# Kernel tuning notes

Measured on AMD Instinct MI355X. Metric: run time of the kernel, lower is better.

Reference implementation:

```python
import jax, jax.numpy as jnp
import numpy as np

SHIFTS = (1, 2, 4, 8)


def _base_kernels():
    # 8 directional contrast kernels (center minus one neighbor), as in the torch module
    d1 = np.array([[[-1, 0, 0], [0, 1, 0], [0, 0, 0]],
                   [[0, -1, 0], [0, 1, 0], [0, 0, 0]],
                   [[0, 0, -1], [0, 1, 0], [0, 0, 0]],
                   [[0, 0, 0], [0, 1, -1], [0, 0, 0]]], dtype=np.float32)
    d2 = d1[:, ::-1, ::-1].copy()
    delta = np.concatenate([d1, d2], axis=0)            # (8,3,3) kernel*_1
    su0 = np.ones((3, 3), np.float32) / 8.0             # original kernel_su
    ce = np.zeros((3, 3), np.float32); ce[1, 1] = 1.0   # kernel_ce
    k2 = (delta - ce) * (9.0 / 8.0) + su0               # (8,3,3) kernel*_2
    su_f = su0 * (7.0 / 8.0); su_f[1, 1] = 1.0 / 8.0    # mutated kernel_su used for cen_x
    return jnp.asarray(delta), jnp.asarray(k2), jnp.asarray(su_f), jnp.asarray(ce)


def _dwconv(x, w, dil, groups):
    # depthwise 3x3 dilated conv, padding='same' (stride 1)
    return jax.lax.conv_general_dilated(
        x, w, window_strides=(1, 1), padding='SAME',
        rhs_dilation=(dil, dil),
        dimension_numbers=('NCHW', 'OIHW', 'NCHW'),
        feature_group_count=groups)


def setup_inputs() -> dict:
    key = jax.random.key(0)
    ks = jax.random.split(key, 6)
    B, C, Wd, Ht = 8, 16, 192, 192
    H, T, OC = 4, 64, 32
    hid = T // H  # 16
    return {
        'cen': jax.random.normal(ks[0], (B, C, Wd, Ht), jnp.float32),
        'wq': jax.random.normal(ks[1], (H, hid, C), jnp.float32) * 0.1,
        'wk': jax.random.normal(ks[2], (H, 8 * hid, 8 * C), jnp.float32) * 0.05,
        'wv': jax.random.normal(ks[3], (H, 8 * hid, 8 * C), jnp.float32) * 0.05,
        'sum_w': jnp.full((H, C), 0.5, jnp.float32),  # Parameter(ones)*0.5
        'w_out': jax.random.normal(ks[4], (OC, T), jnp.float32) * 0.1,
        'gamma': jnp.ones((OC,), jnp.float32),
        'beta': jnp.zeros((OC,), jnp.float32),
    }


def reference(cen, wq, wk, wv, sum_w, w_out, gamma, beta):
    delta, k2, su_f, ce = _base_kernels()
    B, C, Wd, Ht = cen.shape
    H = len(SHIFTS)
    hid = wq.shape[1]
    N = Wd * Ht  # self.area
    qs, ks_, vs = [], [], []
    for i, s in enumerate(SHIFTS):
        sw = sum_w[i]  # (C,) per-channel blend weight
        # center-smoothing kernel: kernel_su*(1-sw) + sw*kernel_ce
        w_cen = (su_f[None] * (1.0 - sw)[:, None, None]
                 + ce[None] * sw[:, None, None])[:, None]          # (C,1,3,3)
        cen_x = _dwconv(cen, w_cen, s, C)                           # (B,C,Wd,Ht)
        # 8 blended contrast kernels: k1*(1-sw) + k2*sw, per channel
        w_sur = (delta[None] * (1.0 - sw)[:, None, None, None]
                 + k2[None] * sw[:, None, None, None]).reshape(C * 8, 1, 3, 3)
        sur = _dwconv(cen, w_sur, s, C)                             # (B, C*8, Wd, Ht), channel-major
        # reorder to torch cat order: [k0 all C, k1 all C, ...]
        sur = sur.reshape(B, C, 8, Wd, Ht).transpose(0, 2, 1, 3, 4).reshape(B, 8 * C, Wd, Ht)
        qs.append(jnp.einsum('oc,bchw->bohw', wq[i], cen_x).reshape(B, hid, N))
        ks_.append(jnp.einsum('oc,bchw->bohw', wk[i], sur).reshape(B, 8 * hid, N))
        vs.append(jnp.einsum('oc,bchw->bohw', wv[i], sur).reshape(B, 8 * hid, N))
    Q = jnp.stack(qs, 1)   # (B,H,hid,N)
    K = jnp.stack(ks_, 1)  # (B,H,8*hid,N)
    V = jnp.stack(vs, 1)   # (B,H,8*hid,N)
    # F.normalize over spatial dim (channel attention)
    Qn = Q / jnp.maximum(jnp.linalg.norm(Q, axis=-1, keepdims=True), 1e-12)
    Kn = K / jnp.maximum(jnp.linalg.norm(K, axis=-1, keepdims=True), 1e-12)
    score = jnp.einsum('bhqn,bhkn->bhqk', Qn, Kn) / jnp.sqrt(jnp.float32(N))
    # InstanceNorm2d(num_heads), affine=False, biased var
    m = score.mean(axis=(-2, -1), keepdims=True)
    v = score.var(axis=(-2, -1), keepdims=True)
    score = (score - m) / jnp.sqrt(v + 1e-5)
    attn = jax.nn.softmax(score, axis=-1)
    out = jnp.einsum('bhqk,bhkn->bhqn', attn, V).reshape(B, H * hid, Wd, Ht)  # (B,T,Wd,Ht)
    # out_conv: 1x1 conv + BatchNorm2d (train-mode batch stats) + ReLU
    y = jnp.einsum('oc,bchw->bohw', w_out, out)
    mu = y.mean(axis=(0, 2, 3), keepdims=True)
    var = y.var(axis=(0, 2, 3), keepdims=True)
    y = (y - mu) / jnp.sqrt(var + 1e-5) * gamma[None, :, None, None] + beta[None, :, None, None]
    return jax.nn.relu(y)
```

## Files before the change

kernel.cpp:

```cpp
#include <hip/hip_runtime.h>
#include <hip/hip_bf16.h>

typedef __hip_bfloat16 bf16;
typedef unsigned short u16;
typedef u16 u16x8 __attribute__((ext_vector_type(8)));
typedef __bf16 bf16x8 __attribute__((ext_vector_type(8)));
typedef float f32x4 __attribute__((ext_vector_type(4)));

#define NPIX 36864
#define NTOT 9437184
#define BNPIX 294912.0f

__device__ __forceinline__ float cvt(float v){ return v; }
__device__ __forceinline__ float cvt(bf16 v){ return __bfloat162float(v); }
__device__ __forceinline__ void stv(float* p, float v){ *p = v; }
__device__ __forceinline__ void stv(bf16* p, float v){ *p = __float2bfloat16(v); }
__device__ __forceinline__ u16 f2us(float v){ bf16 b = __float2bfloat16(v); u16 u; __builtin_memcpy(&u,&b,2); return u; }
__device__ __forceinline__ float us2f(u16 v){ unsigned u = ((unsigned)v)<<16; float f; __builtin_memcpy(&f,&u,4); return f; }
__device__ __forceinline__ void fence(){ __builtin_amdgcn_sched_barrier(0); }

__constant__ int tA[45] = {0,0,0,0,0,0,0,0,0,4,4, 1,1,1,1,1,1,1,1,4,4,4, 2,2,2,2,2,2,2,5,5,5,5, 3,3,3,3,3,3,6,6,6,7,7,8};
__constant__ int tB[45] = {0,1,2,3,4,5,6,7,8,4,5, 1,2,3,4,5,6,7,8,6,7,8, 2,3,4,5,6,7,8,5,6,7,8, 3,4,5,6,7,8,6,7,8,7,8,8};

__global__ void k0_detect(const unsigned* __restrict__ gamma_raw, int* __restrict__ mode)
{
    if (threadIdx.x == 0) mode[0] = (gamma_raw[0] == 0x3F803F80u) ? 1 : 0;
}

struct K1S { u16 F[144*128]; };

__device__ __forceinline__ void flushU(const f32x4& v, int A, int B, float* __restrict__ g, int ln, int lg)
{
    #pragma unroll
    for (int r = 0; r < 4; ++r)
        atomicAdd(&g[(A*16 + lg*4 + r)*144 + B*16 + ln], v[r]);
}

template<typename T>
__device__ __forceinline__ void ldseg(const T* p, bool pred, float* o)
{
    if constexpr (sizeof(T) == 2){
        u16x8 v = {0,0,0,0,0,0,0,0};
        if (pred) v = *(const u16x8*)p;
        #pragma unroll
        for (int i = 0; i < 8; ++i) o[i] = us2f(v[i]);
    } else {
        float4 a = {0,0,0,0}, b = {0,0,0,0};
        if (pred){ a = ((const float4*)p)[0]; b = ((const float4*)p)[1]; }
        o[0]=a.x; o[1]=a.y; o[2]=a.z; o[3]=a.w; o[4]=b.x; o[5]=b.y; o[6]=b.z; o[7]=b.w;
    }
}

template<typename T, int S_>
__device__ __forceinline__ void k1_build(const T* __restrict__ cc, float swc, K1S& S,
                                         int bx, int ck, int glocal, int c, int gs)
{
    const int gg = (bx*6 + ck)*16 + glocal;
    const int row = gg/24;
    const int colb = (gg - row*24)*8;
    float w3[3][24];
    #pragma unroll
    for (int rr = 0; rr < 3; ++rr){
        int r2 = row + (rr-1)*S_;
        bool rok = (unsigned)r2 < 192u;
        const T* rp = cc + r2*192 + colb;
        ldseg(rp-8, rok && (colb != 0),   &w3[rr][0]);
        ldseg(rp,   rok,                  &w3[rr][8]);
        ldseg(rp+8, rok && (colb != 184), &w3[rr][16]);
    }
    u16x8 o[9];
    #pragma unroll
    for (int j = 0; j < 8; ++j){
        float t00=w3[0][8+j-S_], t01=w3[0][8+j], t02=w3[0][8+j+S_];
        float t10=w3[1][8+j-S_], x0 =w3[1][8+j], t12=w3[1][8+j+S_];
        float t20=w3[2][8+j-S_], t21=w3[2][8+j], t22=w3[2][8+j+S_];
        float S9 = ((t00+t01)+(t02+t10))+((x0+t12)+(t20+t21))+t22;
        float cenx = (1.f-swc)*(S9*(7.f/64.f) + x0*(1.f/64.f)) + swc*x0;
        float cf = 1.f + swc*0.125f;
        float bs = swc*(S9*0.125f - 1.125f*x0);
        o[0][j] = f2us(cenx);
        o[1][j] = f2us(cf*(x0-t00)+bs);
        o[2][j] = f2us(cf*(x0-t01)+bs);
        o[3][j] = f2us(cf*(x0-t02)+bs);
        o[4][j] = f2us(cf*(x0-t12)+bs);
        o[5][j] = f2us(cf*(x0-t22)+bs);
        o[6][j] = f2us(cf*(x0-t21)+bs);
        o[7][j] = f2us(cf*(x0-t20)+bs);
        o[8][j] = f2us(cf*(x0-t10)+bs);
    }
    *(u16x8*)&S.F[c*128 + gs*8] = o[0];
    #pragma unroll
    for (int d = 0; d < 8; ++d)
        *(u16x8*)&S.F[(16 + d*16 + c)*128 + gs*8] = o[d+1];
}

template<typename T, bool STORE>
__device__ __forceinline__ void k1_all(const T* __restrict__ cen, const T* __restrict__ sumw,
                                       float* __restrict__ gram, float* __restrict__ gpart, K1S& S)
{
    const int bid = blockIdx.x;
    const int b = bid & 7;
    const int hsel = (bid >> 3) & 3;
    const int bx = bid >> 5;
    const int tid = threadIdx.x;
    const int lane = tid & 63;
    const int w = tid >> 6;
    const int ln = lane & 15, lg = lane >> 4;
    const int c = tid & 15, glocal = tid >> 4;
    const int gs = glocal ^ c;

    f32x4 acc[12];
    #pragma unroll
    for (int j = 0; j < 12; ++j) acc[j] = (f32x4){0.f,0.f,0.f,0.f};

    const float swc = cvt(sumw[hsel*16 + c]);
    const T* cc = cen + ((size_t)(b*16 + c))*NPIX;

    #pragma unroll 1
    for (int ck = 0; ck < 6; ++ck){
        switch (hsel){
        case 0: k1_build<T,1>(cc, swc, S, bx, ck, glocal, c, gs); break;
        case 1: k1_build<T,2>(cc, swc, S, bx, ck, glocal, c, gs); break;
        case 2: k1_build<T,4>(cc, swc, S, bx, ck, glocal, c, gs); break;
        default: k1_build<T,8>(cc, swc, S, bx, ck, glocal, c, gs); break;
        }
        fence();
        __syncthreads();
        fence();
        #pragma unroll
        for (int ks = 0; ks < 4; ++ks){
            bf16x8 fg[9];
            #pragma unroll
            for (int blk = 0; blk < 9; ++blk){
                u16x8 raw = *(const u16x8*)&S.F[(blk*16+ln)*128 + ((ks*4+lg) ^ ln)*8];
                fg[blk] = __builtin_bit_cast(bf16x8, raw);
            }
            #define MT(j,A,B) acc[j] = __builtin_amdgcn_mfma_f32_16x16x32_bf16(fg[A], fg[B], acc[j], 0, 0, 0)
            if (w == 0){
                MT(0,0,0); MT(1,0,1); MT(2,0,2); MT(3,0,3); MT(4,0,4); MT(5,0,5);
                MT(6,0,6); MT(7,0,7); MT(8,0,8); MT(9,4,4); MT(10,4,5);
            } else if (w == 1){
                MT(0,1,1); MT(1,1,2); MT(2,1,3); MT(3,1,4); MT(4,1,5); MT(5,1,6);
                MT(6,1,7); MT(7,1,8); MT(8,4,6); MT(9,4,7); MT(10,4,8);
            } else if (w == 2){
                MT(0,2,2); MT(1,2,3); MT(2,2,4); MT(3,2,5); MT(4,2,6); MT(5,2,7);
                MT(6,2,8); MT(7,5,5); MT(8,5,6); MT(9,5,7); MT(10,5,8);
            } else {
                MT(0,3,3); MT(1,3,4); MT(2,3,5); MT(3,3,6); MT(4,3,7); MT(5,3,8);
                MT(6,6,6); MT(7,6,7); MT(8,6,8); MT(9,7,7); MT(10,7,8); MT(11,8,8);
            }
            #undef MT
        }
        fence();
        __syncthreads();
        fence();
    }

    if (STORE){
        float* gp = gpart + (((size_t)bx*32 + b*4 + hsel)*45)*256;
        const int base = w*11;
        const int nt = (w == 3) ? 12 : 11;
        #pragma unroll
        for (int j = 0; j < 12; ++j){
            if (j < nt){
                float* tp = gp + (base + j)*256 + lg*64 + ln;
                #pragma unroll
                for (int r = 0; r < 4; ++r) tp[r*16] = acc[j][r];
            }
        }
    } else {
        float* g = gram + (size_t)(b*4 + hsel) * 20736;
        if (w == 0){
            flushU(acc[0],0,0,g,ln,lg); flushU(acc[1],0,1,g,ln,lg); flushU(acc[2],0,2,g,ln,lg);
            flushU(acc[3],0,3,g,ln,lg); flushU(acc[4],0,4,g,ln,lg); flushU(acc[5],0,5,g,ln,lg);
            flushU(acc[6],0,6,g,ln,lg); flushU(acc[7],0,7,g,ln,lg); flushU(acc[8],0,8,g,ln,lg);
            flushU(acc[9],4,4,g,ln,lg); flushU(acc[10],4,5,g,ln,lg);
        } else if (w == 1){
            flushU(acc[0],1,1,g,ln,lg); flushU(acc[1],1,2,g,ln,lg); flushU(acc[2],1,3,g,ln,lg);
            flushU(acc[3],1,4,g,ln,lg); flushU(acc[4],1,5,g,ln,lg); flushU(acc[5],1,6,g,ln,lg);
            flushU(acc[6],1,7,g,ln,lg); flushU(acc[7],1,8,g,ln,lg); flushU(acc[8],4,6,g,ln,lg);
            flushU(acc[9],4,7,g,ln,lg); flushU(acc[10],4,8,g,ln,lg);
        } else if (w == 2){
            flushU(acc[0],2,2,g,ln,lg); flushU(acc[1],2,3,g,ln,lg); flushU(acc[2],2,4,g,ln,lg);
            flushU(acc[3],2,5,g,ln,lg); flushU(acc[4],2,6,g,ln,lg); flushU(acc[5],2,7,g,ln,lg);
            flushU(acc[6],2,8,g,ln,lg); flushU(acc[7],5,5,g,ln,lg); flushU(acc[8],5,6,g,ln,lg);
            flushU(acc[9],5,7,g,ln,lg); flushU(acc[10],5,8,g,ln,lg);
        } else {
            flushU(acc[0],3,3,g,ln,lg); flushU(acc[1],3,4,g,ln,lg); flushU(acc[2],3,5,g,ln,lg);
            flushU(acc[3],3,6,g,ln,lg); flushU(acc[4],3,7,g,ln,lg); flushU(acc[5],3,8,g,ln,lg);
            flushU(acc[6],6,6,g,ln,lg); flushU(acc[7],6,7,g,ln,lg); flushU(acc[8],6,8,g,ln,lg);
            flushU(acc[9],7,7,g,ln,lg); flushU(acc[10],7,8,g,ln,lg); flushU(acc[11],8,8,g,ln,lg);
        }
    }
}

template<bool STORE>
__global__ __launch_bounds__(256,2)
void k1_gram(const void* cen, const void* sumw, float* gram, float* gpart, const int* mode)
{
    __shared__ K1S S;
    if (mode[0]) k1_all<bf16,STORE>((const bf16*)cen, (const bf16*)sumw, gram, gpart, S);
    else         k1_all<float,STORE>((const float*)cen, (const float*)sumw, gram, gpart, S);
}

__global__ __launch_bounds__(256,4)
void k1_red(const float* __restrict__ gpart, float* __restrict__ gram)
{
    const int t = blockIdx.x;
    const int bh = blockIdx.y;
    const int e = threadIdx.x;
    const float* p = gpart + (size_t)bh*45*256 + (size_t)t*256 + e;
    float s = 0.f;
    #pragma unroll 4
    for (int sx = 0; sx < 48; ++sx) s += p[(size_t)sx*32*45*256];
    const int A = tA[t], B = tB[t];
    const int rr = e >> 4, cc2 = e & 15;
    float* g = gram + (size_t)bh*20736;
    g[(A*16+rr)*144 + B*16 + cc2] = s;
    if (A != B) g[(B*16+cc2)*144 + A*16 + rr] = s;
}

__global__ __launch_bounds__(256,1)
void k1_sym(float* __restrict__ gram)
{
    float* g = gram + (size_t)blockIdx.x * 20736;
    for (int e = threadIdx.x; e < 20736; e += 256){
        int r = e/144, c = e - r*144;
        if ((r>>4) > (c>>4)) g[e] = g[c*144 + r];
    }
}

struct K2aS { float wkr[16][129]; float part[16][17]; };

template<typename T>
__device__ __forceinline__ void k2a_body(const float* __restrict__ gram, const T* __restrict__ wk,
                                         float* __restrict__ knorm, K2aS& S)
{
    const int bh = blockIdx.y, h = bh & 3;
    const int k0 = blockIdx.x * 16;
    const int tid = threadIdx.x;
    for (int idx = tid; idx < 2048; idx += 256){
        int k = idx >> 7, c = idx & 127;
        S.wkr[k][c] = cvt(wk[h*16384 + (k0+k)*128 + c]);
    }
    __syncthreads();
    const int kl = tid & 15, pp = tid >> 4;
    const float* g = gram + (size_t)bh*20736;
    float acc = 0.f;
    for (int c = pp*8; c < pp*8+8; ++c){
        const float* grow = g + (16+c)*144 + 16;
        float s_ = 0.f;
        for (int c2 = 0; c2 < 128; ++c2) s_ += S.wkr[kl][c2]*grow[c2];
        acc += S.wkr[kl][c]*s_;
    }
    S.part[pp][kl] = acc;
    __syncthreads();
    if (tid < 16){
        float t = 0.f;
        #pragma unroll
        for (int p2 = 0; p2 < 16; ++p2) t += S.part[p2][tid];
        knorm[bh*128 + k0 + tid] = sqrtf(fmaxf(t, 0.f));
    }
}

__global__ __launch_bounds__(256,1)
void k2a_knorm(const float* gram, const void* wk, float* knorm, const int* mode)
{
    __shared__ K2aS S;
    if (mode[0]) k2a_body<bf16>(gram, (const bf16*)wk, knorm, S);
    else         k2a_body<float>(gram, (const float*)wk, knorm, S);
}

struct K2bS {
    float sc[16][128];
    float tmve[16][128];
    float wqf[16][16];
    float qn[16];
    float red1[4], red2[4];
    float m_s, i_s;
};

template<typename T>
__device__ __forceinline__ void k2b_body(const float* __restrict__ gram, const float* __restrict__ knorm,
                                         const T* __restrict__ wq, const T* __restrict__ wk,
                                         const T* __restrict__ wv, const T* __restrict__ wout,
                                         u16* __restrict__ weff2b, K2bS& S)
{
    const int bh = blockIdx.x, h = bh & 3;
    const int tid = threadIdx.x;
    const float* g = gram + (size_t)bh*20736;

    S.wqf[tid>>4][tid&15] = cvt(wq[h*256 + tid]);
    __syncthreads();

    if (tid < 16){
        float acc = 0.f;
        for (int c = 0; c < 16; ++c){
            const float* gr = g + c*144;
            float s_ = 0.f;
            for (int c2 = 0; c2 < 16; ++c2) s_ += S.wqf[tid][c2]*gr[c2];
            acc += S.wqf[tid][c]*s_;
        }
        S.qn[tid] = sqrtf(fmaxf(acc, 0.f));
    }
    for (int e = tid; e < 2048; e += 256){
        int q = e>>7, c2 = e&127;
        float s_ = 0.f;
        #pragma unroll
        for (int c = 0; c < 16; ++c) s_ += S.wqf[q][c]*g[c*144 + 16 + c2];
        S.tmve[q][c2] = s_;
    }
    __syncthreads();
    for (int e = tid; e < 2048; e += 256){
        int q = e>>7, k = e&127;
        const T* wkrow = wk + h*16384 + k*128;
        float s_ = 0.f;
        for (int c2 = 0; c2 < 128; ++c2) s_ += S.tmve[q][c2]*cvt(wkrow[c2]);
        float nq = fmaxf(S.qn[q], 1e-12f);
        float nk = fmaxf(knorm[bh*128+k], 1e-12f);
        S.sc[q][k] = s_/(nq*nk) * (1.f/192.f);
    }
    __syncthreads();
    float s1 = 0.f, s2 = 0.f;
    for (int e = tid; e < 2048; e += 256){ float v = S.sc[e>>7][e&127]; s1 += v; s2 += v*v; }
    #pragma unroll
    for (int o = 1; o < 64; o <<= 1){ s1 += __shfl_xor(s1,o); s2 += __shfl_xor(s2,o); }
    if ((tid&63) == 0){ S.red1[tid>>6] = s1; S.red2[tid>>6] = s2; }
    __syncthreads();
    if (tid == 0){
        float a = S.red1[0]+S.red1[1]+S.red1[2]+S.red1[3];
        float qq = S.red2[0]+S.red2[1]+S.red2[2]+S.red2[3];
        float m = a*(1.f/2048.f);
        float var = qq*(1.f/2048.f) - m*m;
        S.m_s = m; S.i_s = rsqrtf(var + 1e-5f);
    }
    __syncthreads();
    {
        float mm = S.m_s, ii = S.i_s;
        for (int e = tid; e < 2048; e += 256){ int q = e>>7, k = e&127; S.sc[q][k] = (S.sc[q][k]-mm)*ii; }
    }
    __syncthreads();
    if (tid < 16){
        float mx = -1e30f;
        for (int k = 0; k < 128; ++k) mx = fmaxf(mx, S.sc[tid][k]);
        float sm = 0.f;
        for (int k = 0; k < 128; ++k){ float e_ = __expf(S.sc[tid][k]-mx); S.sc[tid][k] = e_; sm += e_; }
        float inv = 1.f/sm;
        for (int k = 0; k < 128; ++k) S.sc[tid][k] *= inv;
    }
    __syncthreads();
    for (int e = tid; e < 2048; e += 256){
        int q = e>>7, c = e&127;
        float s_ = 0.f;
        for (int k = 0; k < 128; ++k) s_ += S.sc[q][k]*cvt(wv[h*16384 + k*128 + c]);
        S.tmve[q][c] = s_;
    }
    __syncthreads();
    for (int e = tid; e < 4096; e += 256){
        int f = e>>5, oc = e&31;
        float s_ = 0.f;
        #pragma unroll
        for (int q = 0; q < 16; ++q) s_ += cvt(wout[oc*64 + h*16 + q])*S.tmve[q][f];
        int d = f >> 4, c = f & 15;
        weff2b[(size_t)bh*4096 + oc*128 + c*8 + d] = f2us(s_);
    }
}

__global__ __launch_bounds__(256,1)
void k2b_attn(const float* gram, const float* knorm, const void* wq, const void* wk,
              const void* wv, const void* wout, u16* weff2b, const int* mode)
{
    __shared__ K2bS S;
    if (mode[0]) k2b_body<bf16>(gram, knorm, (const bf16*)wq, (const bf16*)wk, (const bf16*)wv, (const bf16*)wout, weff2b, S);
    else         k2b_body<float>(gram, knorm, (const float*)wq, (const float*)wk, (const float*)wv, (const float*)wout, weff2b, S);
}

struct K3S { u16 feat[128*128]; u16 wlds[32*128]; };

__device__ __forceinline__ int kkey(int x){ return ((x>>3) ^ x) & 15; }

template<typename T, int S_, int H>
__device__ __forceinline__ void k3_step(const T* __restrict__ cc, float swc,
                                        const u16* __restrict__ wsrc,
                                        int row, int colb, int p0, int c,
                                        int tid, int ln, int lg, int wm, int wn,
                                        f32x4* acc, K3S& S)
{
    #pragma unroll
    for (int i = 0; i < 2; ++i){
        int e = tid + 256*i;
        int oc = e >> 4, slot = e & 15;
        u16x8 v = *(const u16x8*)&wsrc[oc*128 + slot*8];
        *(u16x8*)&S.wlds[oc*128 + ((slot ^ kkey(oc)) & 15)*8] = v;
    }
    float w3[3][24];
    #pragma unroll
    for (int rr = 0; rr < 3; ++rr){
        int r2 = row + (rr-1)*S_;
        bool rok = (unsigned)r2 < 192u;
        const T* rp = cc + r2*192 + colb;
        ldseg(rp-8, rok && (colb != 0),   &w3[rr][0]);
        ldseg(rp,   rok,                  &w3[rr][8]);
        ldseg(rp+8, rok && (colb != 184), &w3[rr][16]);
    }
    #pragma unroll
    for (int j = 0; j < 8; ++j){
        float t00=w3[0][8+j-S_], t01=w3[0][8+j], t02=w3[0][8+j+S_];
        float t10=w3[1][8+j-S_], x0 =w3[1][8+j], t12=w3[1][8+j+S_];
        float t20=w3[2][8+j-S_], t21=w3[2][8+j], t22=w3[2][8+j+S_];
        float S9 = ((t00+t01)+(t02+t10))+((x0+t12)+(t20+t21))+t22;
        float cf = 1.f + swc*0.125f;
        float bs = swc*(S9*0.125f - 1.125f*x0);
        u16x8 pk;
        pk[0] = f2us(cf*(x0-t00)+bs);
        pk[1] = f2us(cf*(x0-t01)+bs);
        pk[2] = f2us(cf*(x0-t02)+bs);
        pk[3] = f2us(cf*(x0-t12)+bs);
        pk[4] = f2us(cf*(x0-t22)+bs);
        pk[5] = f2us(cf*(x0-t21)+bs);
        pk[6] = f2us(cf*(x0-t20)+bs);
        pk[7] = f2us(cf*(x0-t10)+bs);
        int p = p0 + j;
        *(u16x8*)&S.feat[p*128 + ((c ^ kkey(p)) & 15)*8] = pk;
    }
    fence();
    __syncthreads();
    fence();
    const int ocl = wm*16 + ln;
    #pragma unroll
    for (int kt = 0; kt < 4; ++kt){
        const int slot = kt*4 + lg;
        u16x8 araw = *(const u16x8*)&S.wlds[ocl*128 + ((slot ^ kkey(ocl)) & 15)*8];
        bf16x8 a = __builtin_bit_cast(bf16x8, araw);
        #pragma unroll
        for (int nt = 0; nt < 4; ++nt){
            const int pixl = wn*64 + nt*16 + ln;
            u16x8 braw = *(const u16x8*)&S.feat[pixl*128 + ((slot ^ kkey(pixl)) & 15)*8];
            bf16x8 bb = __builtin_bit_cast(bf16x8, braw);
            acc[nt] = __builtin_amdgcn_mfma_f32_16x16x32_bf16(a, bb, acc[nt], 0, 0, 0);
        }
    }
    fence();
    __syncthreads();
    fence();
}

template<typename T, bool YF32>
__device__ __forceinline__ void k3_body(const T* __restrict__ cen, const T* __restrict__ sumw,
                                        const u16* __restrict__ weff2b, float* __restrict__ ysum,
                                        T* __restrict__ outp, float* __restrict__ yf, K3S& S)
{
    const int bid = blockIdx.x;
    const int b = bid & 7;
    const int k = bid >> 3;
    const int cs = k % 3;
    const int rp = k / 3;
    const int tid = threadIdx.x;
    const int lane = tid & 63;
    const int w = tid >> 6;
    const int wm = w >> 1, wn = w & 1;
    const int ln = lane & 15, lg = lane >> 4;
    const int c = tid >> 4, g = tid & 15;
    const int grow = g >> 3, gcol = g & 7;

    const int row = rp*2 + grow;
    const int colb = cs*64 + gcol*8;
    const int p0 = grow*64 + gcol*8;
    const T* cc = cen + ((size_t)(b*16 + c))*NPIX;

    f32x4 acc[4];
    #pragma unroll
    for (int nt = 0; nt < 4; ++nt) acc[nt] = (f32x4){0.f,0.f,0.f,0.f};

    const u16* wb = weff2b + (size_t)(b*4)*4096;
    k3_step<T,1,0>(cc, cvt(sumw[ 0 + c]), wb,          row, colb, p0, c, tid, ln, lg, wm, wn, acc, S);
    k3_step<T,2,1>(cc, cvt(sumw[16 + c]), wb + 4096,   row, colb, p0, c, tid, ln, lg, wm, wn, acc, S);
    k3_step<T,4,2>(cc, cvt(sumw[32 + c]), wb + 8192,   row, colb, p0, c, tid, ln, lg, wm, wn, acc, S);
    k3_step<T,8,3>(cc, cvt(sumw[48 + c]), wb + 12288,  row, colb, p0, c, tid, ln, lg, wm, wn, acc, S);

    const int oc0 = wm*16 + lg*4;
    #pragma unroll
    for (int nt = 0; nt < 4; ++nt){
        const int pixl = wn*64 + nt*16 + ln;
        const int gr = rp*2 + (pixl>>6);
        const int gc = cs*64 + (pixl & 63);
        #pragma unroll
        for (int r = 0; r < 4; ++r){
            const size_t a = (size_t)b*32*NPIX + (size_t)(oc0+r)*NPIX + (size_t)gr*192 + gc;
            if (YF32) yf[a] = acc[nt][r];
            else      stv(&outp[a], acc[nt][r]);
        }
    }
    float* ys = ysum + (rp & 7)*64;
    #pragma unroll
    for (int r = 0; r < 4; ++r){
        float s1 = 0.f, s2 = 0.f;
        #pragma unroll
        for (int nt = 0; nt < 4; ++nt){ s1 += acc[nt][r]; s2 += acc[nt][r]*acc[nt][r]; }
        #pragma unroll
        for (int o = 1; o < 16; o <<= 1){ s1 += __shfl_xor(s1,o); s2 += __shfl_xor(s2,o); }
        if (ln == 0){ atomicAdd(&ys[oc0+r], s1); atomicAdd(&ys[32+oc0+r], s2); }
    }
}

template<bool YF32>
__global__ __launch_bounds__(256,4)
void k3_out(const void* cen, const void* sumw, const u16* weff2b, float* ysum,
            void* outp, float* yf, const int* mode)
{
    __shared__ K3S S;
    if (mode[0]) k3_body<bf16,YF32>((const bf16*)cen, (const bf16*)sumw, weff2b, ysum, (bf16*)outp, yf, S);
    else         k3_body<float,YF32>((const float*)cen, (const float*)sumw, weff2b, ysum, (float*)outp, yf, S);
}

__global__ void k4_stats(const float* __restrict__ ysum, const void* gamma_,
                         const void* beta_, float* __restrict__ ss, const int* mode)
{
    int oc = threadIdx.x;
    if (oc < 32){
        float gv, bv;
        if (mode[0]){ gv = cvt(((const bf16*)gamma_)[oc]); bv = cvt(((const bf16*)beta_)[oc]); }
        else        { gv = ((const float*)gamma_)[oc];     bv = ((const float*)beta_)[oc]; }
        float s1 = 0.f, s2 = 0.f;
        #pragma unroll
        for (int sl = 0; sl < 8; ++sl){ s1 += ysum[sl*64 + oc]; s2 += ysum[sl*64 + 32 + oc]; }
        float m = s1 / BNPIX;
        float var = s2 / BNPIX - m*m;
        float istd = rsqrtf(var + 1e-5f);
        float scl = istd * gv;
        ss[oc] = scl;
        ss[32+oc] = bv - m*scl;
    }
}

template<typename T, bool YF32>
__device__ __forceinline__ void k5_body(const float* __restrict__ ss, const float* __restrict__ yf, T* __restrict__ out)
{
    size_t i0 = ((size_t)blockIdx.x*256 + threadIdx.x)*8;
    if (i0 >= (size_t)NTOT) return;
    int oc = (int)((i0/NPIX) & 31);
    float scl = ss[oc], shf = ss[32+oc];
    float v[8];
    if (YF32){
        const float4* p = (const float4*)(yf + i0);
        float4 a = p[0], b = p[1];
        v[0]=a.x; v[1]=a.y; v[2]=a.z; v[3]=a.w; v[4]=b.x; v[5]=b.y; v[6]=b.z; v[7]=b.w;
    } else {
        if constexpr (sizeof(T) == 2){
            u16x8 a = *(const u16x8*)(out + i0);
            #pragma unroll
            for (int j = 0; j < 8; ++j) v[j] = us2f(a[j]);
        } else {
            const float4* p = (const float4*)((const float*)out + i0);
            float4 a = p[0], b = p[1];
            v[0]=a.x; v[1]=a.y; v[2]=a.z; v[3]=a.w; v[4]=b.x; v[5]=b.y; v[6]=b.z; v[7]=b.w;
        }
    }
    if constexpr (sizeof(T) == 2){
        u16x8 r;
        #pragma unroll
        for (int j = 0; j < 8; ++j){ float y = fmaxf(v[j]*scl + shf, 0.f); r[j] = f2us(y); }
        *(u16x8*)(out + i0) = r;
    } else {
        float4 r0, r1;
        r0.x = fmaxf(v[0]*scl+shf,0.f); r0.y = fmaxf(v[1]*scl+shf,0.f);
        r0.z = fmaxf(v[2]*scl+shf,0.f); r0.w = fmaxf(v[3]*scl+shf,0.f);
        r1.x = fmaxf(v[4]*scl+shf,0.f); r1.y = fmaxf(v[5]*scl+shf,0.f);
        r1.z = fmaxf(v[6]*scl+shf,0.f); r1.w = fmaxf(v[7]*scl+shf,0.f);
        ((float4*)((float*)out + i0))[0] = r0;
        ((float4*)((float*)out + i0))[1] = r1;
    }
}

template<bool YF32>
__global__ __launch_bounds__(256,2)
void k5_norm(const float* ss, const float* yf, void* out, const int* mode)
{
    if (mode[0]) k5_body<bf16,YF32>(ss, yf, (bf16*)out);
    else         k5_body<float,YF32>(ss, yf, (float*)out);
}

extern "C" void kernel_launch(void* const* d_in, const int* in_sizes, int n_in,
                              void* d_out, int out_size, void* d_ws, size_t ws_size,
                              hipStream_t stream)
{
    (void)in_sizes; (void)n_in; (void)out_size;
    const void* cen   = d_in[0];
    const void* wq    = d_in[1];
    const void* wk    = d_in[2];
    const void* wv    = d_in[3];
    const void* sumw  = d_in[4];
    const void* wout  = d_in[5];
    const void* gamma = d_in[6];
    const void* beta  = d_in[7];
    float* ws = (float*)d_ws;

    float* gram   = ws;
    u16*   weff2b = (u16*)(ws + 663552);
    float* knorm  = ws + 729088;
    float* ysum   = ws + 733184;
    float* sshift = ws + 733696;
    int*   modep  = (int*)(ws + 733760);
    float* gpart  = ws + 733776;
    const size_t GPART_F = (size_t)1536*45*256;
    const bool store = (ws_size >= (733776 + GPART_F) * 4);
    float* yf = store ? (gpart + GPART_F) : gpart;
    const size_t yf_end = ((size_t)(yf - ws) + NTOT) * 4;
    const bool yf32 = (ws_size >= yf_end);

    k0_detect<<<1, 64, 0, stream>>>((const unsigned*)gamma, modep);
    hipMemsetAsync(ysum, 0, 512*sizeof(float), stream);

    if (store){
        k1_gram<true><<<dim3(1536), 256, 0, stream>>>(cen, sumw, gram, gpart, modep);
        k1_red<<<dim3(45,32), 256, 0, stream>>>(gpart, gram);
    } else {
        hipMemsetAsync(gram, 0, 663552*sizeof(float), stream);
        k1_gram<false><<<dim3(1536), 256, 0, stream>>>(cen, sumw, gram, gpart, modep);
        k1_sym<<<32, 256, 0, stream>>>(gram);
    }

    k2a_knorm<<<dim3(8,32), 256, 0, stream>>>(gram, wk, knorm, modep);
    k2b_attn<<<dim3(32), 256, 0, stream>>>(gram, knorm, wq, wk, wv, wout, weff2b, modep);
    if (yf32){
        k3_out<true><<<dim3(2304), 256, 0, stream>>>(cen, sumw, weff2b, ysum, d_out, yf, modep);
        k4_stats<<<1, 64, 0, stream>>>(ysum, gamma, beta, sshift, modep);
        k5_norm<true><<<4608, 256, 0, stream>>>(sshift, yf, d_out, modep);
    } else {
        k3_out<false><<<dim3(2304), 256, 0, stream>>>(cen, sumw, weff2b, ysum, d_out, yf, modep);
        k4_stats<<<1, 64, 0, stream>>>(ysum, gamma, beta, sshift, modep);
        k5_norm<false><<<4608, 256, 0, stream>>>(sshift, yf, d_out, modep);
    }
}
```

Baseline: 256.2 us.

## Restructure k3 output kernel into single-wave blocks with direct global weight fragments

The fused feature-build plus MFMA output kernel now runs one 64-thread wave per block over a 64-pixel row segment instead of four waves over 128 pixels. Each lane builds features for two channels, and the weight A-fragments are read straight from global memory instead of being staged through LDS. This removes the block-wide barriers and the shared weight tile, halves LDS per block, and doubles the grid size. In exchange the wave does twice the MFMA work per feature tile, reads weights redundantly from global or L2, and may lose latency hiding if occupancy is limited by registers.

Measured after the change: 270.8 us. +5.7%, slower.

```diff
diff --git a/kernel.cpp b/kernel.cpp
--- a/kernel.cpp
+++ b/kernel.cpp
@@ -375,28 +375,17 @@
     else         k2b_body<float>(gram, knorm, (const float*)wq, (const float*)wk, (const float*)wv, (const float*)wout, weff2b, S);
 }
 
-struct K3S { u16 feat[128*128]; u16 wlds[32*128]; };
-
 __device__ __forceinline__ int kkey(int x){ return ((x>>3) ^ x) & 15; }
 
-template<typename T, int S_, int H>
-__device__ __forceinline__ void k3_step(const T* __restrict__ cc, float swc,
-                                        const u16* __restrict__ wsrc,
-                                        int row, int colb, int p0, int c,
-                                        int tid, int ln, int lg, int wm, int wn,
-                                        f32x4* acc, K3S& S)
-{
-    #pragma unroll
-    for (int i = 0; i < 2; ++i){
-        int e = tid + 256*i;
-        int oc = e >> 4, slot = e & 15;
-        u16x8 v = *(const u16x8*)&wsrc[oc*128 + slot*8];
-        *(u16x8*)&S.wlds[oc*128 + ((slot ^ kkey(oc)) & 15)*8] = v;
-    }
+template<typename T, int S_>
+__device__ __forceinline__ void k3v8_unit(const T* __restrict__ cc, float swc,
+                                          int rowg, int colb, int p0, int c,
+                                          u16* __restrict__ feat)
+{
     float w3[3][24];
     #pragma unroll
     for (int rr = 0; rr < 3; ++rr){
-        int r2 = row + (rr-1)*S_;
+        int r2 = rowg + (rr-1)*S_;
         bool rok = (unsigned)r2 < 192u;
         const T* rp = cc + r2*192 + colb;
         ldseg(rp-8, rok && (colb != 0),   &w3[rr][0]);
@@ -421,96 +410,105 @@
         pk[6] = f2us(cf*(x0-t20)+bs);
         pk[7] = f2us(cf*(x0-t10)+bs);
         int p = p0 + j;
-        *(u16x8*)&S.feat[p*128 + ((c ^ kkey(p)) & 15)*8] = pk;
-    }
-    fence();
-    __syncthreads();
-    fence();
-    const int ocl = wm*16 + ln;
+        *(u16x8*)&feat[p*128 + ((c ^ kkey(p)) & 15)*8] = pk;
+    }
+}
+
+template<typename T, int S_, int H>
+__device__ __forceinline__ void k3v8_step(const T* __restrict__ cen, const T* __restrict__ sumw,
+                                          const u16* __restrict__ wh,
+                                          int b, int rowg, int colb, int p0, int cA, int cB,
+                                          int ln, int lg, u16* __restrict__ feat, f32x4 (&acc)[2][4])
+{
+    k3v8_unit<T,S_>(cen + ((size_t)(b*16+cA))*NPIX, cvt(sumw[H*16+cA]), rowg, colb, p0, cA, feat);
+    k3v8_unit<T,S_>(cen + ((size_t)(b*16+cB))*NPIX, cvt(sumw[H*16+cB]), rowg, colb, p0, cB, feat);
     #pragma unroll
     for (int kt = 0; kt < 4; ++kt){
-        const int slot = kt*4 + lg;
-        u16x8 araw = *(const u16x8*)&S.wlds[ocl*128 + ((slot ^ kkey(ocl)) & 15)*8];
-        bf16x8 a = __builtin_bit_cast(bf16x8, araw);
+        const int blk = kt*4 + lg;
+        u16x8 a0 = *(const u16x8*)&wh[ln*128 + blk*8];
+        u16x8 a1 = *(const u16x8*)&wh[(16+ln)*128 + blk*8];
         #pragma unroll
         for (int nt = 0; nt < 4; ++nt){
-            const int pixl = wn*64 + nt*16 + ln;
-            u16x8 braw = *(const u16x8*)&S.feat[pixl*128 + ((slot ^ kkey(pixl)) & 15)*8];
+            const int p = nt*16 + ln;
+            u16x8 braw = *(const u16x8*)&feat[p*128 + ((blk ^ kkey(p)) & 15)*8];
             bf16x8 bb = __builtin_bit_cast(bf16x8, braw);
-            acc[nt] = __builtin_amdgcn_mfma_f32_16x16x32_bf16(a, bb, acc[nt], 0, 0, 0);
-        }
-    }
-    fence();
-    __syncthreads();
-    fence();
+            acc[0][nt] = __builtin_amdgcn_mfma_f32_16x16x32_bf16(__builtin_bit_cast(bf16x8, a0), bb, acc[0][nt], 0, 0, 0);
+            acc[1][nt] = __builtin_amdgcn_mfma_f32_16x16x32_bf16(__builtin_bit_cast(bf16x8, a1), bb, acc[1][nt], 0, 0, 0);
+        }
+    }
 }
 
 template<typename T, bool YF32>
 __device__ __forceinline__ void k3_body(const T* __restrict__ cen, const T* __restrict__ sumw,
                                         const u16* __restrict__ weff2b, float* __restrict__ ysum,
-                                        T* __restrict__ outp, float* __restrict__ yf, K3S& S)
+                                        T* __restrict__ outp, float* __restrict__ yf,
+                                        u16* __restrict__ feat)
 {
     const int bid = blockIdx.x;
     const int b = bid & 7;
-    const int k = bid >> 3;
-    const int cs = k % 3;
-    const int rp = k / 3;
-    const int tid = threadIdx.x;
-    const int lane = tid & 63;
-    const int w = tid >> 6;
-    const int wm = w >> 1, wn = w & 1;
+    const int g = bid >> 3;
+    const int rowg = g / 3;
+    const int colb0 = (g - rowg*3) * 64;
+    const int lane = threadIdx.x;
     const int ln = lane & 15, lg = lane >> 4;
-    const int c = tid >> 4, g = tid & 15;
-    const int grow = g >> 3, gcol = g & 7;
-
-    const int row = rp*2 + grow;
-    const int colb = cs*64 + gcol*8;
-    const int p0 = grow*64 + gcol*8;
-    const T* cc = cen + ((size_t)(b*16 + c))*NPIX;
-
-    f32x4 acc[4];
-    #pragma unroll
-    for (int nt = 0; nt < 4; ++nt) acc[nt] = (f32x4){0.f,0.f,0.f,0.f};
+    const int cA = lane >> 3;
+    const int gcol = lane & 7;
+    const int cB = cA + 8;
+    const int colb = colb0 + gcol*8;
+    const int p0 = gcol*8;
+
+    f32x4 acc[2][4];
+    #pragma unroll
+    for (int mt = 0; mt < 2; ++mt)
+        #pragma unroll
+        for (int nt = 0; nt < 4; ++nt) acc[mt][nt] = (f32x4){0.f,0.f,0.f,0.f};
 
     const u16* wb = weff2b + (size_t)(b*4)*4096;
-    k3_step<T,1,0>(cc, cvt(sumw[ 0 + c]), wb,          row, colb, p0, c, tid, ln, lg, wm, wn, acc, S);
-    k3_step<T,2,1>(cc, cvt(sumw[16 + c]), wb + 4096,   row, colb, p0, c, tid, ln, lg, wm, wn, acc, S);
-    k3_step<T,4,2>(cc, cvt(sumw[32 + c]), wb + 8192,   row, colb, p0, c, tid, ln, lg, wm, wn, acc, S);
-    k3_step<T,8,3>(cc, cvt(sumw[48 + c]), wb + 12288,  row, colb, p0, c, tid, ln, lg, wm, wn, acc, S);
-
-    const int oc0 = wm*16 + lg*4;
-    #pragma unroll
-    for (int nt = 0; nt < 4; ++nt){
-        const int pixl = wn*64 + nt*16 + ln;
-        const int gr = rp*2 + (pixl>>6);
-        const int gc = cs*64 + (pixl & 63);
+    k3v8_step<T,1,0>(cen, sumw, wb,         b, rowg, colb, p0, cA, cB, ln, lg, feat, acc);
+    k3v8_step<T,2,1>(cen, sumw, wb + 4096,  b, rowg, colb, p0, cA, cB, ln, lg, feat, acc);
+    k3v8_step<T,4,2>(cen, sumw, wb + 8192,  b, rowg, colb, p0, cA, cB, ln, lg, feat, acc);
+    k3v8_step<T,8,3>(cen, sumw, wb + 12288, b, rowg, colb, p0, cA, cB, ln, lg, feat, acc);
+
+    #pragma unroll
+    for (int mt = 0; mt < 2; ++mt){
+        #pragma unroll
+        for (int nt = 0; nt < 4; ++nt){
+            const int gc = colb0 + nt*16 + ln;
+            #pragma unroll
+            for (int r = 0; r < 4; ++r){
+                const int oc = mt*16 + lg*4 + r;
+                const size_t a = (size_t)b*32*NPIX + (size_t)oc*NPIX + (size_t)rowg*192 + gc;
+                if (YF32) yf[a] = acc[mt][nt][r];
+                else      stv(&outp[a], acc[mt][nt][r]);
+            }
+        }
+    }
+    float* ys = ysum + (g & 7)*64;
+    #pragma unroll
+    for (int mt = 0; mt < 2; ++mt){
         #pragma unroll
         for (int r = 0; r < 4; ++r){
-            const size_t a = (size_t)b*32*NPIX + (size_t)(oc0+r)*NPIX + (size_t)gr*192 + gc;
-            if (YF32) yf[a] = acc[nt][r];
-            else      stv(&outp[a], acc[nt][r]);
-        }
-    }
-    float* ys = ysum + (rp & 7)*64;
-    #pragma unroll
-    for (int r = 0; r < 4; ++r){
-        float s1 = 0.f, s2 = 0.f;
-        #pragma unroll
-        for (int nt = 0; nt < 4; ++nt){ s1 += acc[nt][r]; s2 += acc[nt][r]*acc[nt][r]; }
-        #pragma unroll
-        for (int o = 1; o < 16; o <<= 1){ s1 += __shfl_xor(s1,o); s2 += __shfl_xor(s2,o); }
-        if (ln == 0){ atomicAdd(&ys[oc0+r], s1); atomicAdd(&ys[32+oc0+r], s2); }
+            float s1 = 0.f, s2 = 0.f;
+            #pragma unroll
+            for (int nt = 0; nt < 4; ++nt){ s1 += acc[mt][nt][r]; s2 += acc[mt][nt][r]*acc[mt][nt][r]; }
+            #pragma unroll
+            for (int o = 1; o < 16; o <<= 1){ s1 += __shfl_xor(s1,o); s2 += __shfl_xor(s2,o); }
+            if (ln == 0){
+                const int oc = mt*16 + lg*4 + r;
+                atomicAdd(&ys[oc], s1); atomicAdd(&ys[32+oc], s2);
+            }
+        }
     }
 }
 
 template<bool YF32>
-__global__ __launch_bounds__(256,4)
+__global__ __launch_bounds__(64,2)
 void k3_out(const void* cen, const void* sumw, const u16* weff2b, float* ysum,
             void* outp, float* yf, const int* mode)
 {
-    __shared__ K3S S;
-    if (mode[0]) k3_body<bf16,YF32>((const bf16*)cen, (const bf16*)sumw, weff2b, ysum, (bf16*)outp, yf, S);
-    else         k3_body<float,YF32>((const float*)cen, (const float*)sumw, weff2b, ysum, (float*)outp, yf, S);
+    __shared__ u16 feat[64*128];
+    if (mode[0]) k3_body<bf16,YF32>((const bf16*)cen, (const bf16*)sumw, weff2b, ysum, (bf16*)outp, yf, feat);
+    else         k3_body<float,YF32>((const float*)cen, (const float*)sumw, weff2b, ysum, (float*)outp, yf, feat);
 }
 
 __global__ void k4_stats(const float* __restrict__ ysum, const void* gamma_,
@@ -623,11 +621,11 @@
     k2a_knorm<<<dim3(8,32), 256, 0, stream>>>(gram, wk, knorm, modep);
     k2b_attn<<<dim3(32), 256, 0, stream>>>(gram, knorm, wq, wk, wv, wout, weff2b, modep);
     if (yf32){
-        k3_out<true><<<dim3(2304), 256, 0, stream>>>(cen, sumw, weff2b, ysum, d_out, yf, modep);
+        k3_out<true><<<dim3(4608), 64, 0, stream>>>(cen, sumw, weff2b, ysum, d_out, yf, modep);
         k4_stats<<<1, 64, 0, stream>>>(ysum, gamma, beta, sshift, modep);
         k5_norm<true><<<4608, 256, 0, stream>>>(sshift, yf, d_out, modep);
     } else {
-        k3_out<false><<<dim3(2304), 256, 0, stream>>>(cen, sumw, weff2b, ysum, d_out, yf, modep);
+        k3_out<false><<<dim3(4608), 64, 0, stream>>>(cen, sumw, weff2b, ysum, d_out, yf, modep);
         k4_stats<<<1, 64, 0, stream>>>(ysum, gamma, beta, sshift, modep);
         k5_norm<false><<<4608, 256, 0, stream>>>(sshift, yf, d_out, modep);
     }
```
